# Kernel tuning notes

Hardware: AMD Instinct MI355X
Metric: run time of the kernel (lower is better)

The kernel has to match this reference:

```python
import jax, jax.numpy as jnp
import numpy as np

SEQ_LEN = 12          # seq_length
K = 8                 # nsamples = 2 * num_samples
RADII = (4.0 + 1e-06, 8.0 + 1e-06, 12.0 + 1e-06)
COUT = (64, 128, 256)


def _group(xyz, s_xyz, radius):
    # ball query via knn + radius mask: xyz (B,N,3) queries, s_xyz (B,M,3) keys
    d2 = jnp.sum((xyz[:, :, None, :] - s_xyz[:, None, :, :]) ** 2, axis=-1)  # (B,N,M)
    neg, idx = jax.lax.top_k(-d2, K)                                          # (B,N,K)
    valid = (-neg) <= radius * radius
    # points outside the ball are replaced by the nearest neighbor (pad-with-first)
    return jnp.where(valid, idx, idx[..., :1])


def _gather(a, idx):
    # a (B,M,C), idx (B,N,K) -> (B,N,K,C)
    return jax.vmap(lambda t, i: t[i])(a, idx)


def _cell(xyz, feat, state, W, b, radius, cout):
    # PointRNN cell: group state points around current points, fuse
    # [displacement, current feature, state feature] with a shared linear,
    # then max-pool over the K neighbors. New state xyz = current xyz.
    B, N, _ = xyz.shape
    if state is None:
        s_xyz, s_feat = xyz, jnp.zeros((B, N, cout), xyz.dtype)
    else:
        s_xyz, s_feat = state
    idx = _group(xyz, s_xyz, radius)
    n_xyz = _gather(s_xyz, idx)                      # (B,N,K,3)
    n_feat = _gather(s_feat, idx)                    # (B,N,K,cout)
    disp = n_xyz - xyz[:, :, None, :]
    parts = [disp]
    if feat is not None:
        cin = feat.shape[-1]
        parts.append(jnp.broadcast_to(feat[:, :, None, :], (B, N, K, cin)))
    parts.append(n_feat)
    h = jnp.concatenate(parts, axis=-1) @ W + b      # (B,N,K,cout)
    return (xyz, jnp.max(h, axis=2))                 # (xyz, (B,N,cout))


def _forward(frames, W1, b1, W2, b2, W3, b3, Wm, bm, Wl, bl):
    half = SEQ_LEN // 2
    s1 = s2 = s3 = None
    # encode
    for i in range(half):
        s1 = _cell(frames[:, i], None, s1, W1, b1, RADII[0], COUT[0])
        s2 = _cell(s1[0], s1[1], s2, W2, b2, RADII[1], COUT[1])
        s3 = _cell(s2[0], s2[1], s3, W3, b3, RADII[2], COUT[2])
    # decode
    input_frame = frames[:, half - 1]
    preds = []
    for i in range(half, SEQ_LEN):
        s1 = _cell(input_frame, None, s1, W1, b1, RADII[0], COUT[0])
        s2 = _cell(s1[0], s1[1], s2, W2, b2, RADII[1], COUT[1])
        s3 = _cell(s2[0], s2[1], s3, W3, b3, RADII[2], COUT[2])
        h = jax.nn.relu(s3[1] @ Wm + bm)             # MLP([256,64]) = Lin+ReLU
        motion = h @ Wl + bl                         # (B,N,3)
        input_frame = input_frame + motion
        preds.append(input_frame)
    return jnp.stack(preds, axis=1)                  # (B, T/2, N, 3)


def setup_inputs() -> dict:
    key = jax.random.key(0)
    ks = jax.random.split(key, 12)
    B, N = 16, 512
    frames = jax.random.normal(ks[0], (B, SEQ_LEN, N, 3), jnp.float32) * 2.0

    def lin(k, fin, fout):
        k1, k2 = jax.random.split(k)
        s = 1.0 / np.sqrt(fin)
        return (jax.random.uniform(k1, (fin, fout), jnp.float32, -s, s),
                jax.random.uniform(k2, (fout,), jnp.float32, -s, s))

    W1, b1 = lin(ks[1], 3 + 0 + 64, 64)
    W2, b2 = lin(ks[2], 3 + 64 + 128, 128)
    W3, b3 = lin(ks[3], 3 + 128 + 256, 256)
    Wm, bm = lin(ks[4], 256, 64)
    Wl, bl = lin(ks[5], 64, 3)
    return {"frames": frames, "W1": W1, "b1": b1, "W2": W2, "b2": b2,
            "W3": W3, "b3": b3, "Wm": Wm, "bm": bm, "Wl": Wl, "bl": bl}


def reference(frames, W1, b1, W2, b2, W3, b3, Wm, bm, Wl, bl):
    return _forward(frames, W1, b1, W2, b2, W3, b3, Wm, bm, Wl, bl)
```

## Files before the change

### kernel.cpp

```cpp
#include <hip/hip_runtime.h>
#include <hip/hip_cooperative_groups.h>
#include <math.h>

namespace cg = cooperative_groups;

#define BB 16
#define NN 512
#define KNN 8
#define SEQ 12
#define TQK 16
#define QB 32
#define PB 16

typedef __attribute__((ext_vector_type(8))) short bf8_t;
typedef __attribute__((ext_vector_type(4))) float f4_t;

__device__ __forceinline__ ushort f2b(float x) {
    uint u = __float_as_uint(x);
    return (ushort)((u + 0x7fffu + ((u >> 16) & 1u)) >> 16);
}
__device__ __forceinline__ float b2f(ushort h) {
    return __uint_as_float((uint)h << 16);
}

struct CellsSM {
    float s2s[PB][132];
    float s3f[PB][260];
    float dsp[3][PB][KNN][3];
    int   jss[3][PB][KNN];
    union { ushort s1b[2][PB][72]; float hs[PB][64]; } u1;
    ushort s2b[2][PB][136];
    ushort s3c[2][PB][264];
};
union __align__(16) SM {
    CellsSM c;
    ushort  g[256 * 40 + 2 * 128 * 40];
    float   kf[1544 + 4608 + 4608];
};
union __align__(16) GKSM {
    ushort  g[256 * 40 + 2 * 128 * 40];
    float   kf[1544 + 4608 + 4608];
};

#define GRPN 64
__device__ __forceinline__ void group_barrier(int* __restrict__ bar, int g,
                                              int target, int tid) {
    __syncthreads();
    if (tid == 0) {
        __threadfence();
        atomicAdd(&bar[g * 32], 1);
        while (__hip_atomic_load(&bar[g * 32], __ATOMIC_ACQUIRE,
                                 __HIP_MEMORY_SCOPE_AGENT) < target)
            __builtin_amdgcn_s_sleep(2);
        __threadfence();
    }
    __syncthreads();
}

__device__ __forceinline__ void knn512(
        const float* __restrict__ xqp, int xq_bs,
        const float* __restrict__ xsp, int xs_bs,
        int* __restrict__ idx1, int* __restrict__ idx2, int* __restrict__ idx3,
        float r2a, float r2b, float r2c,
        int ntile, int b, float* __restrict__ smf) {
    float* s   = smf;
    float* cdp = smf + 1544;
    int*   cip = (int*)(smf + 1544 + 4608);
    const int tid = threadIdx.x;

    {
        int j = tid;
        const float* p = xsp + (long)b * xs_bs + j * 3;
        int o = 3 * j + (j >> 6);
        s[o + 0] = p[0]; s[o + 1] = p[1]; s[o + 2] = p[2];
    }
    __syncthreads();

    int qi  = tid >> 4;
    int sub = tid & 15;
    int n = ntile * QB + qi;
    const float* q = xqp + (long)b * xq_bs + n * 3;
    float qx = q[0], qy = q[1], qz2 = q[2];

    float bd[KNN];
    int   bi[KNN];
#pragma unroll
    for (int k = 0; k < KNN; ++k) { bd[k] = 1e30f; bi[k] = 0; }

    int j0 = sub * (NN / TQK);
    int sbase = 3 * j0 + (j0 >> 6);
#pragma unroll 4
    for (int jj = 0; jj < NN / TQK; ++jj) {
        float dx = s[sbase + 3 * jj + 0] - qx;
        float dy = s[sbase + 3 * jj + 1] - qy;
        float dz = s[sbase + 3 * jj + 2] - qz2;
        float d2 = fmaf(dx, dx, fmaf(dy, dy, dz * dz));
        if (d2 < bd[KNN - 1]) {
            bd[KNN - 1] = d2; bi[KNN - 1] = j0 + jj;
#pragma unroll
            for (int k = KNN - 1; k >= 1; --k) {
                if (bd[k] < bd[k - 1]) {
                    float td = bd[k]; bd[k] = bd[k - 1]; bd[k - 1] = td;
                    int   ti = bi[k]; bi[k] = bi[k - 1]; bi[k - 1] = ti;
                }
            }
        }
    }

    float* cdq = cdp + (qi * TQK + sub) * (KNN + 1);
    int*   ciq = cip + (qi * TQK + sub) * (KNN + 1);
#pragma unroll
    for (int k = 0; k < KNN; ++k) { cdq[k] = bd[k]; ciq[k] = bi[k]; }
    cdq[KNN] = 1e30f; ciq[KNN] = 0x7fffffff;
    __syncthreads();

    for (int stride = TQK / 2; stride >= 1; stride >>= 1) {
        if (sub < stride) {
            float* ca = cdp + (qi * TQK + sub) * (KNN + 1);
            float* cb = cdp + (qi * TQK + sub + stride) * (KNN + 1);
            int*   ja_p = cip + (qi * TQK + sub) * (KNN + 1);
            int*   jb_p = cip + (qi * TQK + sub + stride) * (KNN + 1);
            float rd[KNN]; int ri[KNN];
            int ia = 0, ib = 0;
#pragma unroll
            for (int k = 0; k < KNN; ++k) {
                float da = ca[ia], db = cb[ib];
                int   ja = ja_p[ia], jb = jb_p[ib];
                bool ta = (da < db) || (da == db && ja < jb);
                rd[k] = ta ? da : db; ri[k] = ta ? ja : jb;
                ia += ta ? 1 : 0; ib += ta ? 0 : 1;
            }
#pragma unroll
            for (int k = 0; k < KNN; ++k) { ca[k] = rd[k]; ja_p[k] = ri[k]; }
        }
        __syncthreads();
    }

    if (sub == 0) {
        long base = ((long)(b * NN + n)) * KNN;
        float* c0  = cdp + qi * TQK * (KNN + 1);
        int*   j0p = cip + qi * TQK * (KNN + 1);
        int i0 = j0p[0];
#pragma unroll
        for (int k = 0; k < KNN; ++k) {
            float d = c0[k]; int j = j0p[k];
            idx1[base + k] = (d <= r2a) ? j : i0;
            idx2[base + k] = (d <= r2b) ? j : i0;
            idx3[base + k] = (d <= r2c) ? j : i0;
        }
    }
}

template<int N, int NC>
__device__ __forceinline__ void gemmTileW(
        const ushort* __restrict__ Ah, const ushort* __restrict__ Al,
        const ushort* __restrict__ Bh, const ushort* __restrict__ Bl,
        ushort* __restrict__ G, int rb, int cb, int tid, ushort* lds) {
    const int row0 = rb * 128, c0 = cb * NC;
    ushort* ah = lds;
    ushort* al = lds + 128 * 40;
    ushort* bh = lds + 256 * 40;
    ushort* bl = lds + 256 * 40 + NC * 40;
    const int wv = tid >> 6, lane = tid & 63;
    const int m = lane & 15, quad = lane >> 4;
    const int lr = tid >> 2, ls = (tid & 3) * 8;

    f4_t acc[NC / 16];
#pragma unroll
    for (int ct = 0; ct < NC / 16; ++ct) acc[ct] = (f4_t){0.f, 0.f, 0.f, 0.f};

    bf8_t pa_h = *(const bf8_t*)(Ah + (long)(row0 + lr) * N + ls);
    bf8_t pa_l = *(const bf8_t*)(Al + (long)(row0 + lr) * N + ls);
    bf8_t pb_h, pb_l;
    const int lrB = (NC == 128) ? lr : (lr & 63);
    if (NC == 128) {
        pb_h = *(const bf8_t*)(Bh + (long)(c0 + lrB) * N + ls);
        pb_l = *(const bf8_t*)(Bl + (long)(c0 + lrB) * N + ls);
    } else {
        const ushort* Bs = (tid < 256) ? Bh : Bl;
        pb_h = *(const bf8_t*)(Bs + (long)(c0 + lrB) * N + ls);
    }

    for (int k0 = 0; k0 < N; k0 += 32) {
        __syncthreads();
        *(bf8_t*)(ah + lr * 40 + ls) = pa_h;
        *(bf8_t*)(al + lr * 40 + ls) = pa_l;
        if (NC == 128) {
            *(bf8_t*)(bh + lrB * 40 + ls) = pb_h;
            *(bf8_t*)(bl + lrB * 40 + ls) = pb_l;
        } else {
            ushort* bs = (tid < 256) ? bh : bl;
            *(bf8_t*)(bs + lrB * 40 + ls) = pb_h;
        }
        __syncthreads();
        if (k0 + 32 < N) {
            int kn = k0 + 32;
            pa_h = *(const bf8_t*)(Ah + (long)(row0 + lr) * N + kn + ls);
            pa_l = *(const bf8_t*)(Al + (long)(row0 + lr) * N + kn + ls);
            if (NC == 128) {
                pb_h = *(const bf8_t*)(Bh + (long)(c0 + lrB) * N + kn + ls);
                pb_l = *(const bf8_t*)(Bl + (long)(c0 + lrB) * N + kn + ls);
            } else {
                const ushort* Bs = (tid < 256) ? Bh : Bl;
                pb_h = *(const bf8_t*)(Bs + (long)(c0 + lrB) * N + kn + ls);
            }
        }
        bf8_t a_h = *(const bf8_t*)(ah + (wv * 16 + m) * 40 + quad * 8);
        bf8_t a_l = *(const bf8_t*)(al + (wv * 16 + m) * 40 + quad * 8);
#pragma unroll
        for (int ct = 0; ct < NC / 16; ++ct) {
            bf8_t bth = *(const bf8_t*)(bh + (ct * 16 + m) * 40 + quad * 8);
            bf8_t btl = *(const bf8_t*)(bl + (ct * 16 + m) * 40 + quad * 8);
            acc[ct] = __builtin_amdgcn_mfma_f32_16x16x32_bf16(a_h, bth, acc[ct], 0, 0, 0);
            acc[ct] = __builtin_amdgcn_mfma_f32_16x16x32_bf16(a_h, btl, acc[ct], 0, 0, 0);
            acc[ct] = __builtin_amdgcn_mfma_f32_16x16x32_bf16(a_l, bth, acc[ct], 0, 0, 0);
        }
    }
#pragma unroll
    for (int ct = 0; ct < NC / 16; ++ct) {
        int col = c0 + ct * 16 + m;
#pragma unroll
        for (int r = 0; r < 4; ++r)
            G[(long)(row0 + wv * 16 + quad * 4 + r) * N + col] = f2b(acc[ct][r]);
    }
}

__device__ __forceinline__ void gemm_dispatch(
        int it, int tid, ushort* lds,
        const ushort* s1h, const ushort* s1l,
        const ushort* s2h, const ushort* s2l,
        const ushort* s3h, const ushort* s3l,
        const ushort* w1h, const ushort* w1l,
        const ushort* w2h, const ushort* w2l,
        const ushort* w3h, const ushort* w3l,
        ushort* G1, ushort* G2, ushort* G3) {
    int g = it & 7, j = it >> 3;
    if (j < 16)
        gemmTileW<256, 128>(s3h, s3l, w3h, w3l, G3, g * 8 + (j & 7), j >> 3,
                            tid, lds);
    else if (j < 24)
        gemmTileW<128, 128>(s2h, s2l, w2h, w2l, G2, g * 8 + (j - 16), 0,
                            tid, lds);
    else
        gemmTileW<64, 64>(s1h, s1l, w1h, w1l, G1, g * 8 + (j - 24), 0,
                          tid, lds);
}

__device__ __forceinline__ void cells_phase(
        bool first,
        const float* __restrict__ xq, int xq_bs,
        const float* __restrict__ xs, int xs_bs,
        const int* __restrict__ i1, const int* __restrict__ i2,
        const int* __restrict__ i3,
        const ushort* __restrict__ G1p, const ushort* __restrict__ G2p,
        const ushort* __restrict__ G3p,
        ushort* __restrict__ s1h, ushort* __restrict__ s1l,
        ushort* __restrict__ s2h, ushort* __restrict__ s2l,
        ushort* __restrict__ s3h, ushort* __restrict__ s3l,
        const float* __restrict__ W1, const float* __restrict__ b1,
        const float* __restrict__ W2, const float* __restrict__ b2,
        const float* __restrict__ W3, const float* __restrict__ b3,
        const ushort* __restrict__ w2fh, const ushort* __restrict__ w2fl,
        const ushort* __restrict__ w3fh, const ushort* __restrict__ w3fl,
        const ushort* __restrict__ wmh, const ushort* __restrict__ wml,
        const float* __restrict__ bm,
        const float* __restrict__ Wl, const float* __restrict__ bl,
        float* __restrict__ xnext, int xn_bs, int do_head,
        int blk, int tid, CellsSM& sm) {
    const int xcd = blk & 7, slot = blk >> 3;
    const int b   = xcd * 2 + (slot >> 5);
    const int n0  = (slot & 31) << 4;
    const long row0 = (long)b * NN + n0;
    const long bN = (long)b * NN;
    const int wv = tid >> 6, lane = tid & 63;
    const int fm = lane & 15, quad = lane >> 4;

    for (int t = tid; t < 3 * PB * KNN; t += 512) {
        int r = t >> 7, rem = t & 127, p = rem >> 3, k = rem & 7;
        const int* ix = (r == 0) ? i1 : ((r == 1) ? i2 : i3);
        int j = ix[(row0 + p) * KNN + k];
        sm.jss[r][p][k] = j;
        const float* sp = xs + (long)b * xs_bs + j * 3;
        const float* qp = xq + (long)b * xq_bs + (n0 + p) * 3;
        sm.dsp[r][p][k][0] = sp[0] - qp[0];
        sm.dsp[r][p][k][1] = sp[1] - qp[1];
        sm.dsp[r][p][k][2] = sp[2] - qp[2];
    }
    __syncthreads();

    {
        int co = tid & 63, q = tid >> 6;
        float g1r[2][KNN];
        if (!first) {
#pragma unroll
            for (int r = 0; r < 2; ++r)
#pragma unroll
                for (int k = 0; k < KNN; ++k)
                    g1r[r][k] = b2f(G1p[(bN + sm.jss[0][2 * q + r][k]) * 64 + co]);
        }
        float wx = W1[co], wy = W1[64 + co], wz = W1[128 + co];
        float bz = b1[co];
#pragma unroll
        for (int r = 0; r < 2; ++r) {
            int p = 2 * q + r;
            float acc = -1e30f;
#pragma unroll
            for (int k = 0; k < KNN; ++k) {
                float v = fmaf(sm.dsp[0][p][k][0], wx, bz);
                v = fmaf(sm.dsp[0][p][k][1], wy, v);
                v = fmaf(sm.dsp[0][p][k][2], wz, v);
                if (!first) v += g1r[r][k];
                acc = fmaxf(acc, v);
            }
            ushort h = f2b(acc);
            ushort l = f2b(acc - b2f(h));
            sm.u1.s1b[0][p][co] = h;
            sm.u1.s1b[1][p][co] = l;
            s1h[(row0 + p) * 64 + co] = h;
            s1l[(row0 + p) * 64 + co] = l;
        }
    }
    __syncthreads();

    float4 g2r[KNN];
    {
        int c4 = tid & 31, g = tid >> 5;
        if (!first) {
#pragma unroll
            for (int k = 0; k < KNN; ++k) {
                ushort4 t = *(const ushort4*)&G2p[(bN + sm.jss[1][g][k]) * 128 + c4 * 4];
                g2r[k] = make_float4(b2f(t.x), b2f(t.y), b2f(t.z), b2f(t.w));
            }
        }
    }

    {
        int col = wv * 16 + fm;
        float bz = b2[col];
        f4_t acc = {bz, bz, bz, bz};
#pragma unroll
        for (int k0 = 0; k0 < 64; k0 += 32) {
            bf8_t ah = *(const bf8_t*)&sm.u1.s1b[0][fm][k0 + quad * 8];
            bf8_t al = *(const bf8_t*)&sm.u1.s1b[1][fm][k0 + quad * 8];
            bf8_t bh = *(const bf8_t*)(w2fh + col * 64 + k0 + quad * 8);
            bf8_t bl = *(const bf8_t*)(w2fl + col * 64 + k0 + quad * 8);
            acc = __builtin_amdgcn_mfma_f32_16x16x32_bf16(ah, bh, acc, 0, 0, 0);
            acc = __builtin_amdgcn_mfma_f32_16x16x32_bf16(ah, bl, acc, 0, 0, 0);
            acc = __builtin_amdgcn_mfma_f32_16x16x32_bf16(al, bh, acc, 0, 0, 0);
        }
#pragma unroll
        for (int r = 0; r < 4; ++r) sm.s2s[quad * 4 + r][col] = acc[r];
    }
    __syncthreads();

    {
        int c4 = tid & 31, g = tid >> 5;
        float4 bse = *(float4*)&sm.s2s[g][c4 * 4];
        float4 wx = ((const float4*)W2)[c4];
        float4 wy = ((const float4*)(W2 + 128))[c4];
        float4 wz = ((const float4*)(W2 + 256))[c4];
        float4 m = make_float4(-1e30f, -1e30f, -1e30f, -1e30f);
#pragma unroll
        for (int k = 0; k < KNN; ++k) {
            float dx = sm.dsp[1][g][k][0], dy = sm.dsp[1][g][k][1],
                  dz = sm.dsp[1][g][k][2];
            float4 v;
            v.x = fmaf(dz, wz.x, fmaf(dy, wy.x, fmaf(dx, wx.x, bse.x)));
            v.y = fmaf(dz, wz.y, fmaf(dy, wy.y, fmaf(dx, wx.y, bse.y)));
            v.z = fmaf(dz, wz.z, fmaf(dy, wy.z, fmaf(dx, wx.z, bse.z)));
            v.w = fmaf(dz, wz.w, fmaf(dy, wy.w, fmaf(dx, wx.w, bse.w)));
            if (!first) {
                v.x += g2r[k].x; v.y += g2r[k].y;
                v.z += g2r[k].z; v.w += g2r[k].w;
            }
            m.x = fmaxf(m.x, v.x); m.y = fmaxf(m.y, v.y);
            m.z = fmaxf(m.z, v.z); m.w = fmaxf(m.w, v.w);
        }
        ushort4 mh, ml;
        mh.x = f2b(m.x); ml.x = f2b(m.x - b2f(mh.x));
        mh.y = f2b(m.y); ml.y = f2b(m.y - b2f(mh.y));
        mh.z = f2b(m.z); ml.z = f2b(m.z - b2f(mh.z));
        mh.w = f2b(m.w); ml.w = f2b(m.w - b2f(mh.w));
        *(ushort4*)&sm.s2b[0][g][c4 * 4] = mh;
        *(ushort4*)&sm.s2b[1][g][c4 * 4] = ml;
        *(ushort4*)&s2h[(row0 + g) * 128 + c4 * 4] = mh;
        *(ushort4*)&s2l[(row0 + g) * 128 + c4 * 4] = ml;
    }
    __syncthreads();

    float4 g3r[2][KNN];
    {
        int c4 = tid & 63, g = tid >> 6;
        if (!first) {
#pragma unroll
            for (int r = 0; r < 2; ++r)
#pragma unroll
                for (int k = 0; k < KNN; ++k) {
                    ushort4 t = *(const ushort4*)&G3p[(bN + sm.jss[2][2 * g + r][k]) * 256 + c4 * 4];
                    g3r[r][k] = make_float4(b2f(t.x), b2f(t.y), b2f(t.z), b2f(t.w));
                }
        }
    }

    {
        int col0 = wv * 16 + fm, col1 = (wv + 8) * 16 + fm;
        float bz0 = b3[col0], bz1 = b3[col1];
        f4_t a0 = {bz0, bz0, bz0, bz0};
        f4_t a1 = {bz1, bz1, bz1, bz1};
#pragma unroll
        for (int k0 = 0; k0 < 128; k0 += 32) {
            bf8_t ah = *(const bf8_t*)&sm.s2b[0][fm][k0 + quad * 8];
            bf8_t al = *(const bf8_t*)&sm.s2b[1][fm][k0 + quad * 8];
            bf8_t b0h = *(const bf8_t*)(w3fh + col0 * 128 + k0 + quad * 8);
            bf8_t b0l = *(const bf8_t*)(w3fl + col0 * 128 + k0 + quad * 8);
            bf8_t b1h = *(const bf8_t*)(w3fh + col1 * 128 + k0 + quad * 8);
            bf8_t b1l = *(const bf8_t*)(w3fl + col1 * 128 + k0 + quad * 8);
            a0 = __builtin_amdgcn_mfma_f32_16x16x32_bf16(ah, b0h, a0, 0, 0, 0);
            a0 = __builtin_amdgcn_mfma_f32_16x16x32_bf16(ah, b0l, a0, 0, 0, 0);
            a0 = __builtin_amdgcn_mfma_f32_16x16x32_bf16(al, b0h, a0, 0, 0, 0);
            a1 = __builtin_amdgcn_mfma_f32_16x16x32_bf16(ah, b1h, a1, 0, 0, 0);
            a1 = __builtin_amdgcn_mfma_f32_16x16x32_bf16(ah, b1l, a1, 0, 0, 0);
            a1 = __builtin_amdgcn_mfma_f32_16x16x32_bf16(al, b1h, a1, 0, 0, 0);
        }
#pragma unroll
        for (int r = 0; r < 4; ++r) {
            sm.s3f[quad * 4 + r][col0] = a0[r];
            sm.s3f[quad * 4 + r][col1] = a1[r];
        }
    }
    __syncthreads();

    {
        int c4 = tid & 63, g = tid >> 6;
        float4 wx = ((const float4*)W3)[c4];
        float4 wy = ((const float4*)(W3 + 256))[c4];
        float4 wz = ((const float4*)(W3 + 512))[c4];
#pragma unroll
        for (int r = 0; r < 2; ++r) {
            int p = 2 * g + r;
            float4 bse = *(float4*)&sm.s3f[p][c4 * 4];
            float4 m = make_float4(-1e30f, -1e30f, -1e30f, -1e30f);
#pragma unroll
            for (int k = 0; k < KNN; ++k) {
                float dx = sm.dsp[2][p][k][0], dy = sm.dsp[2][p][k][1],
                      dz = sm.dsp[2][p][k][2];
                float4 v;
                v.x = fmaf(dz, wz.x, fmaf(dy, wy.x, fmaf(dx, wx.x, bse.x)));
                v.y = fmaf(dz, wz.y, fmaf(dy, wy.y, fmaf(dx, wx.y, bse.y)));
                v.z = fmaf(dz, wz.z, fmaf(dy, wy.z, fmaf(dx, wx.z, bse.z)));
                v.w = fmaf(dz, wz.w, fmaf(dy, wy.w, fmaf(dx, wx.w, bse.w)));
                if (!first) {
                    v.x += g3r[r][k].x; v.y += g3r[r][k].y;
                    v.z += g3r[r][k].z; v.w += g3r[r][k].w;
                }
                m.x = fmaxf(m.x, v.x); m.y = fmaxf(m.y, v.y);
                m.z = fmaxf(m.z, v.z); m.w = fmaxf(m.w, v.w);
            }
            ushort4 mh, ml;
            mh.x = f2b(m.x); ml.x = f2b(m.x - b2f(mh.x));
            mh.y = f2b(m.y); ml.y = f2b(m.y - b2f(mh.y));
            mh.z = f2b(m.z); ml.z = f2b(m.z - b2f(mh.z));
            mh.w = f2b(m.w); ml.w = f2b(m.w - b2f(mh.w));
            *(ushort4*)&sm.s3c[0][p][c4 * 4] = mh;
            *(ushort4*)&sm.s3c[1][p][c4 * 4] = ml;
            *(ushort4*)&s3h[(row0 + p) * 256 + c4 * 4] = mh;
            *(ushort4*)&s3l[(row0 + p) * 256 + c4 * 4] = ml;
        }
    }

    if (do_head) {
        __syncthreads();
        if (wv < 4) {
            int col = wv * 16 + fm;
            float bz = bm[col];
            f4_t acc = {bz, bz, bz, bz};
#pragma unroll
            for (int k0 = 0; k0 < 256; k0 += 32) {
                bf8_t ah = *(const bf8_t*)&sm.s3c[0][fm][k0 + quad * 8];
                bf8_t al = *(const bf8_t*)&sm.s3c[1][fm][k0 + quad * 8];
                bf8_t bh = *(const bf8_t*)(wmh + col * 256 + k0 + quad * 8);
                bf8_t bl = *(const bf8_t*)(wml + col * 256 + k0 + quad * 8);
                acc = __builtin_amdgcn_mfma_f32_16x16x32_bf16(ah, bh, acc, 0, 0, 0);
                acc = __builtin_amdgcn_mfma_f32_16x16x32_bf16(ah, bl, acc, 0, 0, 0);
                acc = __builtin_amdgcn_mfma_f32_16x16x32_bf16(al, bh, acc, 0, 0, 0);
            }
            __syncthreads();
#pragma unroll
            for (int r = 0; r < 4; ++r)
                sm.u1.hs[quad * 4 + r][col] = fmaxf(acc[r], 0.f);
        } else {
            __syncthreads();
        }
        __syncthreads();
        if (tid < PB * 3) {
            int p = tid / 3, d = tid % 3;
            float m = bl[d];
#pragma unroll 4
            for (int c = 0; c < 64; ++c)
                m = fmaf(sm.u1.hs[p][c], Wl[c * 3 + d], m);
            const float* qp = xq + (long)b * xq_bs + (n0 + p) * 3;
            xnext[(long)b * xn_bs + (n0 + p) * 3 + d] = qp[d] + m;
        }
    }
}

__device__ __forceinline__ void convW_one(int id,
        const float* __restrict__ W1, const float* __restrict__ W2,
        const float* __restrict__ W3, const float* __restrict__ Wm,
        ushort* w1h, ushort* w1l, ushort* w2h, ushort* w2l,
        ushort* w3h, ushort* w3l, ushort* w2fh, ushort* w2fl,
        ushort* w3fh, ushort* w3fl, ushort* wmh, ushort* wml) {
    float v; ushort* ph; ushort* pl; int idx;
    if (id < 4096)        { int n = id >> 6, k = id & 63;
        v = W1[(3 + k) * 64 + n];   ph = w1h;  pl = w1l;  idx = id; }
    else if (id < 20480)  { int u = id - 4096, n = u >> 7, k = u & 127;
        v = W2[(67 + k) * 128 + n]; ph = w2h;  pl = w2l;  idx = u; }
    else if (id < 86016)  { int u = id - 20480, n = u >> 8, k = u & 255;
        v = W3[(131 + k) * 256 + n]; ph = w3h; pl = w3l;  idx = u; }
    else if (id < 94208)  { int u = id - 86016, n = u >> 6, k = u & 63;
        v = W2[(3 + k) * 128 + n];  ph = w2fh; pl = w2fl; idx = u; }
    else if (id < 126976) { int u = id - 94208, n = u >> 7, k = u & 127;
        v = W3[(3 + k) * 256 + n];  ph = w3fh; pl = w3fl; idx = u; }
    else if (id < 143360) { int u = id - 126976, n = u >> 8, k = u & 255;
        v = Wm[k * 64 + n];         ph = wmh;  pl = wml;  idx = u; }
    else return;
    ushort h = f2b(v);
    ph[idx] = h; pl[idx] = f2b(v - b2f(h));
}

__global__ __launch_bounds__(512, 4) void fused_kernel(
        const float* frames, float* out,
        ushort* G1, ushort* G2, ushort* G3,
        ushort* s1h, ushort* s1l, ushort* s2h, ushort* s2l,
        ushort* s3h, ushort* s3l,
        ushort* w1h, ushort* w1l, ushort* w2h, ushort* w2l,
        ushort* w3h, ushort* w3l,
        ushort* w2fh, ushort* w2fl, ushort* w3fh, ushort* w3fl,
        ushort* wmh, ushort* wml,
        int* idx1w, int* idx2w, int* idx3w, int* bar,
        const float* W1, const float* b1, const float* W2, const float* b2,
        const float* W3, const float* b3, const float* Wm, const float* bm,
        const float* Wl, const float* bl,
        float r2a, float r2b, float r2c) {
    __shared__ SM sm;
    cg::grid_group grid = cg::this_grid();
    const int bx = blockIdx.x, tid = threadIdx.x;
    const int grp = bx & 7;
    const int FB = SEQ * NN * 3, OB = 6 * NN * 3;
    const long BNK = (long)BB * NN * KNN;

    if (bx == 0 && tid < 8) bar[tid * 32] = 0;
    convW_one(bx * 512 + tid, W1, W2, W3, Wm,
              w1h, w1l, w2h, w2l, w3h, w3l,
              w2fh, w2fl, w3fh, w3fl, wmh, wml);
    if (bx < 256) {
        int xcd = bx & 7, slot = bx >> 3;
        int b = xcd * 2 + (slot & 1), ntile = slot >> 1;
        knn512(frames, FB, frames, FB, idx1w, idx2w, idx3w,
               r2a, r2b, r2c, ntile, b, sm.kf);
    }
    __threadfence();
    grid.sync();

    int ph = 1;

    for (int t = 0; t < SEQ; ++t) {
        const float* xq; int xq_bs; const float* xs; int xs_bs;
        if (t < 6)       { xq = frames + (long)t * NN * 3;        xq_bs = FB; }
        else if (t == 6) { xq = frames + 5L * NN * 3;             xq_bs = FB; }
        else             { xq = out + (long)(t - 7) * NN * 3;     xq_bs = OB; }
        if (t == 0)      { xs = xq;                               xs_bs = xq_bs; }
        else if (t <= 6) { xs = frames + (long)(t - 1) * NN * 3;  xs_bs = FB; }
        else if (t == 7) { xs = frames + 5L * NN * 3;             xs_bs = FB; }
        else             { xs = out + (long)(t - 8) * NN * 3;     xs_bs = OB; }
        int slot = (t <= 6) ? t : 0;
        const int* i1 = idx1w + slot * BNK;
        const int* i2 = idx2w + slot * BNK;
        const int* i3 = idx3w + slot * BNK;
        int do_head = (t >= 6);
        float* xnext = do_head ? out + (long)(t - 6) * NN * 3 : nullptr;

        cells_phase(t == 0, xq, xq_bs, xs, xs_bs, i1, i2, i3,
                    G1, G2, G3, s1h, s1l, s2h, s2l, s3h, s3l,
                    W1, b1, W2, b2, W3, b3,
                    w2fh, w2fl, w3fh, w3fl, wmh, wml, bm,
                    Wl, bl, xnext, OB, do_head, bx, tid, sm.c);

        if (t == SEQ - 1) break;
        group_barrier(bar, grp, GRPN * ph, tid); ++ph;

        if (bx < 256) {
            int tn = t + 1;
            const float* kq; int kq_bs; const float* ksp; int ks_bs; int kslot;
            if (tn <= 6) {
                int qz = tn < 5 ? tn : 5;
                kq = frames + (long)qz * NN * 3;        kq_bs = FB;
                ksp = frames + (long)(tn - 1) * NN * 3; ks_bs = FB;
                kslot = tn;
            } else {
                kq = out + (long)(tn - 7) * NN * 3;     kq_bs = OB;
                if (tn == 7) { ksp = frames + 5L * NN * 3;          ks_bs = FB; }
                else         { ksp = out + (long)(tn - 8) * NN * 3; ks_bs = OB; }
                kslot = 0;
            }
            int xcd = bx & 7, slot2 = bx >> 3;
            int b = xcd * 2 + (slot2 & 1), ntile = slot2 >> 1;
            knn512(kq, kq_bs, ksp, ks_bs,
                   idx1w + (long)kslot * BNK, idx2w + (long)kslot * BNK,
                   idx3w + (long)kslot * BNK,
                   r2a, r2b, r2c, ntile, b, sm.kf);
        } else {
            gemm_dispatch(bx - 256, tid, sm.g,
                          s1h, s1l, s2h, s2l, s3h, s3l,
                          w1h, w1l, w2h, w2l, w3h, w3l, G1, G2, G3);
        }
        group_barrier(bar, grp, GRPN * ph, tid); ++ph;
    }
}

__global__ __launch_bounds__(512) void init512_kernel(
        const float* __restrict__ frames, int FB,
        int* __restrict__ i1, int* __restrict__ i2, int* __restrict__ i3,
        float r2a, float r2b, float r2c,
        const float* __restrict__ W1, const float* __restrict__ W2,
        const float* __restrict__ W3, const float* __restrict__ Wm,
        ushort* w1h, ushort* w1l, ushort* w2h, ushort* w2l,
        ushort* w3h, ushort* w3l, ushort* w2fh, ushort* w2fl,
        ushort* w3fh, ushort* w3fl, ushort* wmh, ushort* wml) {
    __shared__ float kf[1544 + 4608 + 4608];
    int bx = blockIdx.x;
    if (bx < 256) {
        int xcd = bx & 7, slot = bx >> 3;
        int b = xcd * 2 + (slot & 1), ntile = slot >> 1;
        knn512(frames, FB, frames, FB, i1, i2, i3, r2a, r2b, r2c,
               ntile, b, kf);
        return;
    }
    convW_one((bx - 256) * 512 + threadIdx.x, W1, W2, W3, Wm,
              w1h, w1l, w2h, w2l, w3h, w3l,
              w2fh, w2fl, w3fh, w3fl, wmh, wml);
}

__global__ __launch_bounds__(512) void cells512_kernel(
        int first,
        const float* __restrict__ xq, int xq_bs,
        const float* __restrict__ xs, int xs_bs,
        const int* __restrict__ i1, const int* __restrict__ i2,
        const int* __restrict__ i3,
        const ushort* __restrict__ G1p, const ushort* __restrict__ G2p,
        const ushort* __restrict__ G3p,
        ushort* s1h, ushort* s1l, ushort* s2h, ushort* s2l,
        ushort* s3h, ushort* s3l,
        const float* __restrict__ W1, const float* __restrict__ b1,
        const float* __restrict__ W2, const float* __restrict__ b2,
        const float* __restrict__ W3, const float* __restrict__ b3,
        const ushort* __restrict__ w2fh, const ushort* __restrict__ w2fl,
        const ushort* __restrict__ w3fh, const ushort* __restrict__ w3fl,
        const ushort* __restrict__ wmh, const ushort* __restrict__ wml,
        const float* __restrict__ bm,
        const float* __restrict__ Wl, const float* __restrict__ bl,
        float* xnext, int xn_bs, int do_head) {
    __shared__ CellsSM sm;
    cells_phase(first != 0, xq, xq_bs, xs, xs_bs, i1, i2, i3,
                G1p, G2p, G3p, s1h, s1l, s2h, s2l, s3h, s3l,
                W1, b1, W2, b2, W3, b3, w2fh, w2fl, w3fh, w3fl,
                wmh, wml, bm, Wl, bl, xnext, xn_bs, do_head,
                blockIdx.x, threadIdx.x, sm);
}

__global__ __launch_bounds__(512) void gemmknn512_kernel(
        const ushort* s1h, const ushort* s1l,
        const ushort* s2h, const ushort* s2l,
        const ushort* s3h, const ushort* s3l,
        const ushort* w1h, const ushort* w1l,
        const ushort* w2h, const ushort* w2l,
        const ushort* w3h, const ushort* w3l,
        ushort* G1, ushort* G2, ushort* G3,
        const float* __restrict__ kq, int kq_bs,
        const float* __restrict__ ks, int ks_bs,
        int* ki1, int* ki2, int* ki3,
        float r2a, float r2b, float r2c) {
    __shared__ GKSM sm;
    int bx = blockIdx.x, tid = threadIdx.x;
    if (bx < 256) {
        int xcd = bx & 7, slot = bx >> 3;
        int b = xcd * 2 + (slot & 1), ntile = slot >> 1;
        knn512(kq, kq_bs, ks, ks_bs, ki1, ki2, ki3, r2a, r2b, r2c,
               ntile, b, sm.kf);
        return;
    }
    gemm_dispatch(bx - 256, tid, sm.g,
                  s1h, s1l, s2h, s2l, s3h, s3l,
                  w1h, w1l, w2h, w2l, w3h, w3l, G1, G2, G3);
}

extern "C" void kernel_launch(void* const* d_in, const int* in_sizes, int n_in,
                              void* d_out, int out_size, void* d_ws, size_t ws_size,
                              hipStream_t stream) {
    const float* frames = (const float*)d_in[0];
    const float* W1 = (const float*)d_in[1]; const float* b1 = (const float*)d_in[2];
    const float* W2 = (const float*)d_in[3]; const float* b2 = (const float*)d_in[4];
    const float* W3 = (const float*)d_in[5]; const float* b3 = (const float*)d_in[6];
    const float* Wm = (const float*)d_in[7]; const float* bm = (const float*)d_in[8];
    const float* Wl = (const float*)d_in[9]; const float* bl = (const float*)d_in[10];
    float* out = (float*)d_out;

    const long M = (long)BB * NN;
    ushort* us = (ushort*)d_ws;
    ushort* G1b = us; us += M * 64;
    ushort* G2b = us; us += M * 128;
    ushort* G3b = us; us += M * 256;
    ushort* s1h = us; us += M * 64;   ushort* s1l = us; us += M * 64;
    ushort* s2h = us; us += M * 128;  ushort* s2l = us; us += M * 128;
    ushort* s3h = us; us += M * 256;  ushort* s3l = us; us += M * 256;
    ushort* w1h = us; us += 4096;     ushort* w1l = us; us += 4096;
    ushort* w2h = us; us += 16384;    ushort* w2l = us; us += 16384;
    ushort* w3h = us; us += 65536;    ushort* w3l = us; us += 65536;
    ushort* w2fh = us; us += 8192;    ushort* w2fl = us; us += 8192;
    ushort* w3fh = us; us += 32768;   ushort* w3fl = us; us += 32768;
    ushort* wmh = us; us += 16384;    ushort* wml = us; us += 16384;
    us += (size_t)us & 1;
    const long BNK = M * KNN;
    int* ip = (int*)us;
    int* idx1w = ip; ip += 7 * BNK;
    int* idx2w = ip; ip += 7 * BNK;
    int* idx3w = ip; ip += 7 * BNK;
    int* bar   = ip; ip += 8 * 32;

    double ra = 4.0 + 1e-6, rbd = 8.0 + 1e-6, rc = 12.0 + 1e-6;
    float r2a = (float)(ra * ra), r2b = (float)(rbd * rbd), r2c = (float)(rc * rc);

    const int FB = SEQ * NN * 3;
    const int OB = 6 * NN * 3;

    static int g_coop = -1;
    if (g_coop < 0) {
        int attr = 0, dev = 0, nb = 0;
        hipGetDevice(&dev);
        hipDeviceGetAttribute(&attr, hipDeviceAttributeCooperativeLaunch, dev);
        hipDeviceProp_t prop{};
        hipGetDeviceProperties(&prop, dev);
        if (attr &&
            hipOccupancyMaxActiveBlocksPerMultiprocessor(
                &nb, fused_kernel, 512, 0) == hipSuccess &&
            nb * prop.multiProcessorCount >= 512)
            g_coop = 1;
        else
            g_coop = 0;
    }

    bool did_coop = false;
    if (g_coop == 1) {
        void* args[] = {
            (void*)&frames, (void*)&out,
            (void*)&G1b, (void*)&G2b, (void*)&G3b,
            (void*)&s1h, (void*)&s1l, (void*)&s2h, (void*)&s2l,
            (void*)&s3h, (void*)&s3l,
            (void*)&w1h, (void*)&w1l, (void*)&w2h, (void*)&w2l,
            (void*)&w3h, (void*)&w3l,
            (void*)&w2fh, (void*)&w2fl, (void*)&w3fh, (void*)&w3fl,
            (void*)&wmh, (void*)&wml,
            (void*)&idx1w, (void*)&idx2w, (void*)&idx3w, (void*)&bar,
            (void*)&W1, (void*)&b1, (void*)&W2, (void*)&b2,
            (void*)&W3, (void*)&b3, (void*)&Wm, (void*)&bm,
            (void*)&Wl, (void*)&bl,
            (void*)&r2a, (void*)&r2b, (void*)&r2c
        };
        hipError_t e = hipLaunchCooperativeKernel((const void*)fused_kernel,
                                                  dim3(512), dim3(512),
                                                  args, 0, stream);
        did_coop = (e == hipSuccess);
        if (!did_coop) g_coop = 0;
    }

    if (!did_coop) {
        init512_kernel<<<536, 512, 0, stream>>>(
            frames, FB, idx1w, idx2w, idx3w, r2a, r2b, r2c,
            W1, W2, W3, Wm, w1h, w1l, w2h, w2l, w3h, w3l,
            w2fh, w2fl, w3fh, w3fl, wmh, wml);

        for (int t = 0; t < SEQ; ++t) {
            const float* xq; int xq_bs; const float* xs; int xs_bs;
            if (t < 6)       { xq = frames + (long)t * NN * 3;        xq_bs = FB; }
            else if (t == 6) { xq = frames + 5L * NN * 3;             xq_bs = FB; }
            else             { xq = out + (long)(t - 7) * NN * 3;     xq_bs = OB; }
            if (t == 0)      { xs = xq;                               xs_bs = xq_bs; }
            else if (t <= 6) { xs = frames + (long)(t - 1) * NN * 3;  xs_bs = FB; }
            else if (t == 7) { xs = frames + 5L * NN * 3;             xs_bs = FB; }
            else             { xs = out + (long)(t - 8) * NN * 3;     xs_bs = OB; }

            int slot = (t <= 6) ? t : 0;
            int* i1 = idx1w + (long)slot * BNK;
            int* i2 = idx2w + (long)slot * BNK;
            int* i3 = idx3w + (long)slot * BNK;

            int do_head = (t >= 6);
            float* xnext = do_head ? out + (long)(t - 6) * NN * 3 : nullptr;

            cells512_kernel<<<BB * NN / PB, 512, 0, stream>>>(
                t == 0 ? 1 : 0, xq, xq_bs, xs, xs_bs, i1, i2, i3,
                G1b, G2b, G3b, s1h, s1l, s2h, s2l, s3h, s3l,
                W1, b1, W2, b2, W3, b3,
                w2fh, w2fl, w3fh, w3fl, wmh, wml, bm,
                Wl, bl, xnext, OB, do_head);

            if (t < SEQ - 1) {
                int tn = t + 1;
                const float* kq; int kq_bs; const float* ksp; int ks_bs; int kslot;
                if (tn <= 6) {
                    int qz = tn < 5 ? tn : 5;
                    kq = frames + (long)qz * NN * 3;        kq_bs = FB;
                    ksp = frames + (long)(tn - 1) * NN * 3; ks_bs = FB;
                    kslot = tn;
                } else {
                    kq = out + (long)(tn - 7) * NN * 3;     kq_bs = OB;
                    if (tn == 7) { ksp = frames + 5L * NN * 3;          ks_bs = FB; }
                    else         { ksp = out + (long)(tn - 8) * NN * 3; ks_bs = OB; }
                    kslot = 0;
                }
                gemmknn512_kernel<<<512, 512, 0, stream>>>(
                    s1h, s1l, s2h, s2l, s3h, s3l,
                    w1h, w1l, w2h, w2l, w3h, w3l,
                    G1b, G2b, G3b,
                    kq, kq_bs, ksp, ks_bs,
                    idx1w + (long)kslot * BNK, idx2w + (long)kslot * BNK,
                    idx3w + (long)kslot * BNK,
                    r2a, r2b, r2c);
            }
        }
    }
}
```

Measured before the change: 521.6 us.

## Replace fences in group barriers with system-scope relaxed atomic loads/stores

Removes the __threadfence calls and acquire semantics from the inter-block group barrier. Instead, every cross-block producer/consumer access (state buffers, GEMM outputs, kNN indices, predicted frames) becomes a relaxed system-scope atomic load or store, which bypasses non-coherent caches. GEMM and state stores are also packed into 32-bit pairs through lane shuffles. This aims to cut the cost of fences at each barrier, but it relies on relaxed ordering being sufficient and adds uncached traffic on the gathers, so it risks both correctness and slower memory access.

```diff
diff --git a/kernel.cpp b/kernel.cpp
--- a/kernel.cpp
+++ b/kernel.cpp
@@ -14,6 +14,7 @@
 
 typedef __attribute__((ext_vector_type(8))) short bf8_t;
 typedef __attribute__((ext_vector_type(4))) float f4_t;
+typedef unsigned long long ull;
 
 __device__ __forceinline__ ushort f2b(float x) {
     uint u = __float_as_uint(x);
@@ -21,6 +22,42 @@
 }
 __device__ __forceinline__ float b2f(ushort h) {
     return __uint_as_float((uint)h << 16);
+}
+
+__device__ __forceinline__ uint ld_sys32(const ushort* p) {
+    return __hip_atomic_load((const uint*)p, __ATOMIC_RELAXED,
+                             __HIP_MEMORY_SCOPE_SYSTEM);
+}
+__device__ __forceinline__ ull ld_sys64(const void* p) {
+    return __hip_atomic_load((const ull*)p, __ATOMIC_RELAXED,
+                             __HIP_MEMORY_SCOPE_SYSTEM);
+}
+__device__ __forceinline__ int ld_sysi(const int* p) {
+    return __hip_atomic_load(p, __ATOMIC_RELAXED, __HIP_MEMORY_SCOPE_SYSTEM);
+}
+__device__ __forceinline__ void st_sys32(ushort* p, uint v) {
+    __hip_atomic_store((uint*)p, v, __ATOMIC_RELAXED,
+                       __HIP_MEMORY_SCOPE_SYSTEM);
+}
+__device__ __forceinline__ void st_sys64(void* p, ull v) {
+    __hip_atomic_store((ull*)p, v, __ATOMIC_RELAXED,
+                       __HIP_MEMORY_SCOPE_SYSTEM);
+}
+__device__ __forceinline__ void st_sysi(int* p, int v) {
+    __hip_atomic_store(p, v, __ATOMIC_RELAXED, __HIP_MEMORY_SCOPE_SYSTEM);
+}
+__device__ __forceinline__ void st_sysf(float* p, float v) {
+    __hip_atomic_store(p, v, __ATOMIC_RELAXED, __HIP_MEMORY_SCOPE_SYSTEM);
+}
+__device__ __forceinline__ void st_sys_u4(ushort* p, ushort4 v) {
+    union { ushort4 s; ull u; } c; c.s = v;
+    st_sys64(p, c.u);
+}
+__device__ __forceinline__ bf8_t ld_sys_b128(const ushort* p) {
+    union { ull u[2]; bf8_t v; } c;
+    c.u[0] = ld_sys64(p);
+    c.u[1] = ld_sys64(p + 4);
+    return c.v;
 }
 
 struct CellsSM {
@@ -47,12 +84,11 @@
                                               int target, int tid) {
     __syncthreads();
     if (tid == 0) {
-        __threadfence();
-        atomicAdd(&bar[g * 32], 1);
-        while (__hip_atomic_load(&bar[g * 32], __ATOMIC_ACQUIRE,
-                                 __HIP_MEMORY_SCOPE_AGENT) < target)
-            __builtin_amdgcn_s_sleep(2);
-        __threadfence();
+        __hip_atomic_fetch_add(&bar[g * 32], 1, __ATOMIC_RELAXED,
+                               __HIP_MEMORY_SCOPE_SYSTEM);
+        while (__hip_atomic_load(&bar[g * 32], __ATOMIC_RELAXED,
+                                 __HIP_MEMORY_SCOPE_SYSTEM) < target)
+            __builtin_amdgcn_s_sleep(4);
     }
     __syncthreads();
 }
@@ -144,9 +180,9 @@
 #pragma unroll
         for (int k = 0; k < KNN; ++k) {
             float d = c0[k]; int j = j0p[k];
-            idx1[base + k] = (d <= r2a) ? j : i0;
-            idx2[base + k] = (d <= r2b) ? j : i0;
-            idx3[base + k] = (d <= r2c) ? j : i0;
+            st_sysi(&idx1[base + k], (d <= r2a) ? j : i0);
+            st_sysi(&idx2[base + k], (d <= r2b) ? j : i0);
+            st_sysi(&idx3[base + k], (d <= r2c) ? j : i0);
         }
     }
 }
@@ -169,8 +205,8 @@
 #pragma unroll
     for (int ct = 0; ct < NC / 16; ++ct) acc[ct] = (f4_t){0.f, 0.f, 0.f, 0.f};
 
-    bf8_t pa_h = *(const bf8_t*)(Ah + (long)(row0 + lr) * N + ls);
-    bf8_t pa_l = *(const bf8_t*)(Al + (long)(row0 + lr) * N + ls);
+    bf8_t pa_h = ld_sys_b128(Ah + (long)(row0 + lr) * N + ls);
+    bf8_t pa_l = ld_sys_b128(Al + (long)(row0 + lr) * N + ls);
     bf8_t pb_h, pb_l;
     const int lrB = (NC == 128) ? lr : (lr & 63);
     if (NC == 128) {
@@ -195,8 +231,8 @@
         __syncthreads();
         if (k0 + 32 < N) {
             int kn = k0 + 32;
-            pa_h = *(const bf8_t*)(Ah + (long)(row0 + lr) * N + kn + ls);
-            pa_l = *(const bf8_t*)(Al + (long)(row0 + lr) * N + kn + ls);
+            pa_h = ld_sys_b128(Ah + (long)(row0 + lr) * N + kn + ls);
+            pa_l = ld_sys_b128(Al + (long)(row0 + lr) * N + kn + ls);
             if (NC == 128) {
                 pb_h = *(const bf8_t*)(Bh + (long)(c0 + lrB) * N + kn + ls);
                 pb_l = *(const bf8_t*)(Bl + (long)(c0 + lrB) * N + kn + ls);
@@ -220,8 +256,13 @@
     for (int ct = 0; ct < NC / 16; ++ct) {
         int col = c0 + ct * 16 + m;
 #pragma unroll
-        for (int r = 0; r < 4; ++r)
-            G[(long)(row0 + wv * 16 + quad * 4 + r) * N + col] = f2b(acc[ct][r]);
+        for (int r = 0; r < 4; ++r) {
+            ushort v = f2b(acc[ct][r]);
+            ushort vn = (ushort)__shfl_down((int)v, 1);
+            if (!(m & 1))
+                st_sys32(G + (long)(row0 + wv * 16 + quad * 4 + r) * N + col,
+                         (uint)v | ((uint)vn << 16));
+        }
     }
 }
 
@@ -278,7 +319,7 @@
     for (int t = tid; t < 3 * PB * KNN; t += 512) {
         int r = t >> 7, rem = t & 127, p = rem >> 3, k = rem & 7;
         const int* ix = (r == 0) ? i1 : ((r == 1) ? i2 : i3);
-        int j = ix[(row0 + p) * KNN + k];
+        int j = ld_sysi(&ix[(row0 + p) * KNN + k]);
         sm.jss[r][p][k] = j;
         const float* sp = xs + (long)b * xs_bs + j * 3;
         const float* qp = xq + (long)b * xq_bs + (n0 + p) * 3;
@@ -295,8 +336,12 @@
 #pragma unroll
             for (int r = 0; r < 2; ++r)
 #pragma unroll
-                for (int k = 0; k < KNN; ++k)
-                    g1r[r][k] = b2f(G1p[(bN + sm.jss[0][2 * q + r][k]) * 64 + co]);
+                for (int k = 0; k < KNN; ++k) {
+                    uint vv = ld_sys32(G1p + (bN + sm.jss[0][2 * q + r][k]) * 64
+                                       + (co & ~1));
+                    ushort hv = (co & 1) ? (ushort)(vv >> 16) : (ushort)vv;
+                    g1r[r][k] = b2f(hv);
+                }
         }
         float wx = W1[co], wy = W1[64 + co], wz = W1[128 + co];
         float bz = b1[co];
@@ -316,8 +361,12 @@
             ushort l = f2b(acc - b2f(h));
             sm.u1.s1b[0][p][co] = h;
             sm.u1.s1b[1][p][co] = l;
-            s1h[(row0 + p) * 64 + co] = h;
-            s1l[(row0 + p) * 64 + co] = l;
+            ushort hn = (ushort)__shfl_down((int)h, 1);
+            ushort ln = (ushort)__shfl_down((int)l, 1);
+            if (!(co & 1)) {
+                st_sys32(s1h + (row0 + p) * 64 + co, (uint)h | ((uint)hn << 16));
+                st_sys32(s1l + (row0 + p) * 64 + co, (uint)l | ((uint)ln << 16));
+            }
         }
     }
     __syncthreads();
@@ -328,8 +377,9 @@
         if (!first) {
 #pragma unroll
             for (int k = 0; k < KNN; ++k) {
-                ushort4 t = *(const ushort4*)&G2p[(bN + sm.jss[1][g][k]) * 128 + c4 * 4];
-                g2r[k] = make_float4(b2f(t.x), b2f(t.y), b2f(t.z), b2f(t.w));
+                ull v = ld_sys64(&G2p[(bN + sm.jss[1][g][k]) * 128 + c4 * 4]);
+                g2r[k] = make_float4(b2f((ushort)v), b2f((ushort)(v >> 16)),
+                                     b2f((ushort)(v >> 32)), b2f((ushort)(v >> 48)));
             }
         }
     }
@@ -383,8 +433,8 @@
         mh.w = f2b(m.w); ml.w = f2b(m.w - b2f(mh.w));
         *(ushort4*)&sm.s2b[0][g][c4 * 4] = mh;
         *(ushort4*)&sm.s2b[1][g][c4 * 4] = ml;
-        *(ushort4*)&s2h[(row0 + g) * 128 + c4 * 4] = mh;
-        *(ushort4*)&s2l[(row0 + g) * 128 + c4 * 4] = ml;
+        st_sys_u4(&s2h[(row0 + g) * 128 + c4 * 4], mh);
+        st_sys_u4(&s2l[(row0 + g) * 128 + c4 * 4], ml);
     }
     __syncthreads();
 
@@ -396,8 +446,9 @@
             for (int r = 0; r < 2; ++r)
 #pragma unroll
                 for (int k = 0; k < KNN; ++k) {
-                    ushort4 t = *(const ushort4*)&G3p[(bN + sm.jss[2][2 * g + r][k]) * 256 + c4 * 4];
-                    g3r[r][k] = make_float4(b2f(t.x), b2f(t.y), b2f(t.z), b2f(t.w));
+                    ull v = ld_sys64(&G3p[(bN + sm.jss[2][2 * g + r][k]) * 256 + c4 * 4]);
+                    g3r[r][k] = make_float4(b2f((ushort)v), b2f((ushort)(v >> 16)),
+                                            b2f((ushort)(v >> 32)), b2f((ushort)(v >> 48)));
                 }
         }
     }
@@ -463,8 +514,8 @@
             mh.w = f2b(m.w); ml.w = f2b(m.w - b2f(mh.w));
             *(ushort4*)&sm.s3c[0][p][c4 * 4] = mh;
             *(ushort4*)&sm.s3c[1][p][c4 * 4] = ml;
-            *(ushort4*)&s3h[(row0 + p) * 256 + c4 * 4] = mh;
-            *(ushort4*)&s3l[(row0 + p) * 256 + c4 * 4] = ml;
+            st_sys_u4(&s3h[(row0 + p) * 256 + c4 * 4], mh);
+            st_sys_u4(&s3l[(row0 + p) * 256 + c4 * 4], ml);
         }
     }
 
@@ -499,7 +550,7 @@
             for (int c = 0; c < 64; ++c)
                 m = fmaf(sm.u1.hs[p][c], Wl[c * 3 + d], m);
             const float* qp = xq + (long)b * xq_bs + (n0 + p) * 3;
-            xnext[(long)b * xn_bs + (n0 + p) * 3 + d] = qp[d] + m;
+            st_sysf(&xnext[(long)b * xn_bs + (n0 + p) * 3 + d], qp[d] + m);
         }
     }
 }
@@ -549,7 +600,7 @@
     const int FB = SEQ * NN * 3, OB = 6 * NN * 3;
     const long BNK = (long)BB * NN * KNN;
 
-    if (bx == 0 && tid < 8) bar[tid * 32] = 0;
+    if (bx == 0 && tid < 8) st_sysi(&bar[tid * 32], 0);
     convW_one(bx * 512 + tid, W1, W2, W3, Wm,
               w1h, w1l, w2h, w2l, w3h, w3l,
               w2fh, w2fl, w3fh, w3fl, wmh, wml);
@@ -559,7 +610,6 @@
         knn512(frames, FB, frames, FB, idx1w, idx2w, idx3w,
                r2a, r2b, r2c, ntile, b, sm.kf);
     }
-    __threadfence();
     grid.sync();
 
     int ph = 1;
```

Measured after the change: 510.9 us (median of 2 runs). 2.1% less time.
